# Performance work log

Measured on AMD Instinct MI355X. Metric: run time of the kernel, lower is better.

The kernel has to match this reference:

```python
import jax, jax.numpy as jnp
import numpy as np

LABEL_SIZE = 32
HIDDEN = 1024
TARGET = 1  # args.target
N_EVENTS = 4096
N_SIM = 4096


def setup_inputs() -> dict:
    key = jax.random.key(0)
    ks = jax.random.split(key, 10)
    L, H, n, n_sim = LABEL_SIZE, HIDDEN, N_EVENTS, N_SIM
    label_seq = jax.random.randint(ks[0], (n,), 0, L + 1)
    # strictly increasing event times (positive gaps)
    gaps = jax.random.uniform(ks[1], (n,), minval=0.01, maxval=1.0)
    time_seq = jnp.cumsum(gaps)
    sim_time_idx = jax.random.randint(ks[2], (n_sim,), 0, n - 1)
    sim_time_seq = time_seq[sim_time_idx] + jax.random.uniform(ks[3], (n_sim,), minval=0.0, maxval=0.5)
    stdv = 1.0 / np.sqrt(H)
    u = lambda k, shape: jax.random.uniform(k, shape, minval=-stdv, maxval=stdv)
    Emb = u(ks[4], (H, L + 1))
    W = u(ks[5], (7, H, H))
    U = u(ks[6], (7, H, H))
    d = jnp.zeros((7, H), dtype=jnp.float32)
    w = u(ks[7], (L, H))
    log_s = jnp.zeros((L,), dtype=jnp.float32)
    return {"label_seq": label_seq, "time_seq": time_seq, "sim_time_seq": sim_time_seq,
            "sim_time_idx": sim_time_idx, "ignore_first": 1,
            "Emb": Emb, "W": W, "U": U, "d": d, "w": w, "log_s": log_s}


def _neg_loglik(label_seq, time_seq, sim_time_seq, sim_time_idx, ignore_first,
                Emb, W, U, d, w, log_s):
    H = Emb.shape[0]
    tgt = TARGET
    emb = Emb[:, label_seq].T              # (n, H) event-label embeddings
    # Precompute input-to-gate projections for all steps: W @ label_prev
    Wx = jnp.einsum('ehk,nk->neh', W, emb[:-1])   # (n-1, 7, H)
    dts = time_seq[1:] - time_seq[:-1]            # (n-1,)

    def step(carry, inp):
        c_t, h_t, c_bar = carry
        wx, dt = inp
        temp = wx + jnp.einsum('ehk,k->eh', U, h_t) + d   # (7, H)
        i_g = jax.nn.sigmoid(temp[0])
        f_g = jax.nn.sigmoid(temp[1])
        z = jnp.tanh(temp[2])
        o = jax.nn.sigmoid(temp[3])
        i_b = jax.nn.sigmoid(temp[4])
        f_b = jax.nn.sigmoid(temp[5])
        delta = jax.nn.softplus(temp[6])
        c = f_g * c_t + i_g * z
        c_bar_n = f_b * c_bar + i_b * z
        c_t_n = c_bar_n + (c - c_bar_n) * jnp.exp(-delta * dt)
        h_n = o * jnp.tanh(c_t_n)
        return (c_t_n, h_n, c_bar_n), (h_n, c_bar_n, c, delta, o)

    z0 = jnp.zeros((H,), dtype=time_seq.dtype)
    _, (all_h, all_cbar, all_c, all_delta, all_o) = jax.lax.scan(step, (z0, z0, z0), (Wx, dts))

    def h_to_lambd(h):
        s = jnp.exp(log_s)
        return s * jax.nn.softplus((h @ w.T) / s) + 1e-9

    beg = 1 if ignore_first else 0
    h_evt = all_h[beg:-1]                               # (n-2-beg, H)
    lambd = h_to_lambd(h_evt)                           # (n-2-beg, L)
    mask = label_seq[1 + beg:-1] == tgt
    term1 = jnp.sum(jnp.where(mask, jnp.log(lambd[:, tgt - 1]), 0.0))

    decay = jnp.exp(-all_delta[sim_time_idx] * (sim_time_seq - time_seq[sim_time_idx])[:, None])
    c_sim = all_cbar[sim_time_idx] + (all_c[sim_time_idx] - all_cbar[sim_time_idx]) * decay
    h_sim = all_o[sim_time_idx] * jnp.tanh(c_sim)
    lambd_sim = h_to_lambd(h_sim)
    term2 = jnp.mean(lambd_sim[:, tgt - 1]) * (time_seq[-1] - time_seq[0])
    return -(term1 - term2)


def reference(label_seq, time_seq, sim_time_seq, sim_time_idx, ignore_first, Emb, W, U, d, w, log_s):
    return _neg_loglik(label_seq, time_seq, sim_time_seq, sim_time_idx, ignore_first,
                       Emb, W, U, d, w, log_s)
```

## Files before the change

kernel.cpp:

```cpp
#include <hip/hip_runtime.h>
#include <math.h>

#define H      1024
#define LBLP1  33
#define NE     4096
#define NS     4096
#define NSTEP  (NE - 1)
#define TGT    1
#define NWG    256
#define UPW    4
#define ROWS   28
#define SCAN_THREADS 512
#define SENTINEL 0xFFFFFFFFu

__device__ __forceinline__ float wave_sum(float v) {
#pragma unroll
    for (int o = 32; o > 0; o >>= 1) v += __shfl_xor(v, o, 64);
    return v;
}

__device__ __forceinline__ float softplusf(float x) {
    return x > 0.f ? x + log1pf(expf(-x)) : log1pf(expf(x));
}
__device__ __forceinline__ float sigmoidf(float x) {
    return 1.f / (1.f + expf(-x));
}

__global__ void embT_kernel(const float* __restrict__ Emb, float* __restrict__ EmbT) {
    int l = blockIdx.x;
    for (int k = threadIdx.x; k < H; k += blockDim.x)
        EmbT[(size_t)l * H + k] = Emb[(size_t)k * LBLP1 + l];
}

__global__ void wemb_kernel(const float* __restrict__ W, const float* __restrict__ EmbT,
                            const float* __restrict__ dbias, float* __restrict__ WEmb) {
    int row  = blockIdx.x;
    int wave = threadIdx.x >> 6;
    int lane = threadIdx.x & 63;
    __shared__ float wrow[H];
    for (int i = threadIdx.x; i < H; i += blockDim.x) wrow[i] = W[(size_t)row * H + i];
    __syncthreads();
    float db = dbias[row];
    for (int l = wave; l < LBLP1; l += 4) {
        const float* ec = EmbT + (size_t)l * H;
        float a = 0.f;
#pragma unroll
        for (int m = 0; m < 16; ++m) {
            int k = lane + (m << 6);
            a = fmaf(wrow[k], ec[k], a);
        }
        a = wave_sum(a);
        if (lane == 0) WEmb[(size_t)row * LBLP1 + l] = a + db;
    }
}

__global__ __launch_bounds__(SCAN_THREADS)
void scan_kernel(const float* __restrict__ WEmb, const float* __restrict__ U,
                 const int* __restrict__ label_seq, const float* __restrict__ time_seq,
                 float* __restrict__ all_h, float* __restrict__ all_o,
                 float* __restrict__ all_cb, float* __restrict__ all_cc,
                 float* __restrict__ all_dl) {
    const int tid  = threadIdx.x;
    const int wg   = blockIdx.x;
    const int wave = tid >> 6;
    const int lane = tid & 63;

    extern __shared__ float smem[];
    float* Uld    = smem;
    float* h_sh   = Uld + ROWS * H;
    float* act_sh = h_sh + H;
    float* wes    = act_sh + 32;

    for (int idx = tid; idx < ROWS * H; idx += SCAN_THREADS) {
        int r = idx >> 10, k = idx & (H - 1);
        int e = r >> 2, j = r & 3;
        Uld[idx] = U[((size_t)e * H + (wg * UPW + j)) * H + k];
    }
    for (int idx = tid; idx < ROWS * LBLP1; idx += SCAN_THREADS) {
        int r = idx / LBLP1, l = idx - r * LBLP1;
        int e = r >> 2, j = r & 3;
        wes[idx] = WEmb[((size_t)e * H + (wg * UPW + j)) * LBLP1 + l];
    }
    __syncthreads();

    float c_t = 0.f, cbar = 0.f;
    const float4* h4 = (const float4*)h_sh;

    for (int t = 0; t < NSTEP; ++t) {
        const int   lab = label_seq[t];
        const float dt  = time_seq[t + 1] - time_seq[t];
        float gb[4];
#pragma unroll
        for (int i = 0; i < 4; ++i) {
            int r = wave + (i << 3);
            gb[i] = (r < ROWS) ? wes[r * LBLP1 + lab] : 0.f;
        }

        if (wave == 0) {
            union { unsigned u[16]; float4 f[4]; } cv;
            if (t > 0) {
                const unsigned* src =
                    (const unsigned*)(all_h + (size_t)(t - 1) * H) + (lane << 4);
                for (;;) {
                    bool ok = true;
#pragma unroll
                    for (int j = 0; j < 16; ++j)
                        cv.u[j] = __hip_atomic_load(src + j, __ATOMIC_RELAXED,
                                                    __HIP_MEMORY_SCOPE_AGENT);
#pragma unroll
                    for (int j = 0; j < 16; ++j) ok &= (cv.u[j] != SENTINEL);
                    if (ok) break;
                }
            } else {
#pragma unroll
                for (int j = 0; j < 4; ++j) cv.f[j] = make_float4(0.f, 0.f, 0.f, 0.f);
            }
            float4* dst = (float4*)h_sh + (lane << 2);
#pragma unroll
            for (int j = 0; j < 4; ++j) dst[j] = cv.f[j];
        }
        __syncthreads();

        float4 hr[4];
#pragma unroll
        for (int m = 0; m < 4; ++m) hr[m] = h4[(m << 6) + lane];

#pragma unroll
        for (int i = 0; i < 4; ++i) {
            int r = wave + (i << 3);
            if (r < ROWS) {
                const float4* u4 = (const float4*)(Uld + (r << 10));
                float a = 0.f;
#pragma unroll
                for (int m = 0; m < 4; ++m) {
                    float4 u = u4[(m << 6) + lane];
                    a = fmaf(u.x, hr[m].x, a); a = fmaf(u.y, hr[m].y, a);
                    a = fmaf(u.z, hr[m].z, a); a = fmaf(u.w, hr[m].w, a);
                }
                a = wave_sum(a);
                if (lane == 0) {
                    float g = gb[i] + a;
                    int e = r >> 2;
                    float act;
                    if (e == 2)      act = tanhf(g);
                    else if (e == 6) act = softplusf(g);
                    else             act = sigmoidf(g);
                    act_sh[r] = act;
                }
            }
        }
        __syncthreads();

        if (tid < UPW) {
            float i_g = act_sh[tid],      f_g = act_sh[4 + tid];
            float z   = act_sh[8 + tid],  o   = act_sh[12 + tid];
            float i_b = act_sh[16 + tid], f_b = act_sh[20 + tid];
            float dl  = act_sh[24 + tid];
            float c   = fmaf(f_g, c_t, i_g * z);
            float cbn = fmaf(f_b, cbar, i_b * z);
            float ctn = cbn + (c - cbn) * expf(-dl * dt);
            float hn  = o * tanhf(ctn);
            c_t = ctn; cbar = cbn;
            size_t p = (size_t)t * H + wg * UPW + tid;
            __hip_atomic_store(&all_h[p], hn, __ATOMIC_RELAXED, __HIP_MEMORY_SCOPE_AGENT);
            all_o [p] = o;
            all_cb[p] = cbn;
            all_cc[p] = c;
            all_dl[p] = dl;
        }
    }
}

__global__ void term1_kernel(const float* __restrict__ all_h, const int* __restrict__ label_seq,
                             const float* __restrict__ w, const float* __restrict__ log_s,
                             const int* __restrict__ ignore_first, float* __restrict__ acc) {
    int beg = (*ignore_first) ? 1 : 0;
    int j = blockIdx.x;
    if (j >= (NSTEP - 1 - beg)) return;
    if (label_seq[1 + beg + j] != TGT) return;
    const float* hrow = all_h + (size_t)(beg + j) * H;
    const float* w0 = w + (TGT - 1) * H;
    float part = 0.f;
    for (int i = threadIdx.x; i < H; i += blockDim.x) part += hrow[i] * w0[i];
    __shared__ float red[4];
    part = wave_sum(part);
    if ((threadIdx.x & 63) == 0) red[threadIdx.x >> 6] = part;
    __syncthreads();
    if (threadIdx.x == 0) {
        float tot = red[0] + red[1] + red[2] + red[3];
        float s0 = expf(log_s[TGT - 1]);
        float lam = s0 * softplusf(tot / s0) + 1e-9f;
        atomicAdd(acc, logf(lam));
    }
}

__global__ void term2_kernel(const float* __restrict__ all_o, const float* __restrict__ all_cb,
                             const float* __restrict__ all_cc, const float* __restrict__ all_dl,
                             const int* __restrict__ sim_idx, const float* __restrict__ sim_time,
                             const float* __restrict__ time_seq, const float* __restrict__ w,
                             const float* __restrict__ log_s, float* __restrict__ acc) {
    int i = blockIdx.x;
    int idx = sim_idx[i];
    float dtp = sim_time[i] - time_seq[idx];
    size_t base = (size_t)idx * H;
    const float* w0 = w + (TGT - 1) * H;
    float part = 0.f;
    for (int hh = threadIdx.x; hh < H; hh += blockDim.x) {
        float cb = all_cb[base + hh];
        float cc = all_cc[base + hh];
        float dl = all_dl[base + hh];
        float oo = all_o [base + hh];
        float cs = cb + (cc - cb) * expf(-dl * dtp);
        part += oo * tanhf(cs) * w0[hh];
    }
    __shared__ float red[4];
    part = wave_sum(part);
    if ((threadIdx.x & 63) == 0) red[threadIdx.x >> 6] = part;
    __syncthreads();
    if (threadIdx.x == 0) {
        float tot = red[0] + red[1] + red[2] + red[3];
        float s0 = expf(log_s[TGT - 1]);
        float lam = s0 * softplusf(tot / s0) + 1e-9f;
        atomicAdd(acc + 1, lam);
    }
}

__global__ void finish_kernel(const float* __restrict__ acc, const float* __restrict__ time_seq,
                              float* __restrict__ out) {
    float T = time_seq[NE - 1] - time_seq[0];
    out[0] = -(acc[0] - acc[1] * (T / (float)NS));
}

extern "C" void kernel_launch(void* const* d_in, const int* in_sizes, int n_in,
                              void* d_out, int out_size, void* d_ws, size_t ws_size,
                              hipStream_t stream) {
    const int*   label_seq    = (const int*)  d_in[0];
    const float* time_seq     = (const float*)d_in[1];
    const float* sim_time     = (const float*)d_in[2];
    const int*   sim_idx      = (const int*)  d_in[3];
    const int*   ignore_first = (const int*)  d_in[4];
    const float* Emb   = (const float*)d_in[5];
    const float* W     = (const float*)d_in[6];
    const float* U     = (const float*)d_in[7];
    const float* dbias = (const float*)d_in[8];
    const float* w     = (const float*)d_in[9];
    const float* log_s = (const float*)d_in[10];
    float* out = (float*)d_out;

    float* ws = (float*)d_ws;
    size_t off = 0;
    float* acc    = ws + off;  off += 32;
    float* EmbT   = ws + off;  off += (size_t)LBLP1 * H;
    float* WEmb   = ws + off;  off += 7 * H * LBLP1;
    off = (off + 3) & ~(size_t)3;
    float* all_h  = ws + off;  off += (size_t)NSTEP * H;
    float* all_o  = ws + off;  off += (size_t)NSTEP * H;
    float* all_cb = ws + off;  off += (size_t)NSTEP * H;
    float* all_cc = ws + off;  off += (size_t)NSTEP * H;
    float* all_dl = ws + off;  off += (size_t)NSTEP * H;

    hipMemsetAsync(acc, 0, 2 * sizeof(float), stream);
    hipMemsetAsync(all_h, 0xFF, (size_t)NSTEP * H * sizeof(float), stream);

    hipLaunchKernelGGL(embT_kernel, dim3(LBLP1), dim3(256), 0, stream, Emb, EmbT);
    hipLaunchKernelGGL(wemb_kernel, dim3(7 * H), dim3(256), 0, stream,
                       W, EmbT, dbias, WEmb);

    unsigned int smem_bytes = (unsigned int)((ROWS * H + H + 32 + ROWS * LBLP1) * sizeof(float));
    hipFuncSetAttribute((const void*)scan_kernel, hipFuncAttributeMaxDynamicSharedMemorySize,
                        (int)smem_bytes);
    void* args[] = { (void*)&WEmb, (void*)&U, (void*)&label_seq, (void*)&time_seq,
                     (void*)&all_h, (void*)&all_o, (void*)&all_cb, (void*)&all_cc,
                     (void*)&all_dl };
    hipLaunchCooperativeKernel((void*)scan_kernel, dim3(NWG), dim3(SCAN_THREADS),
                               args, smem_bytes, stream);

    hipLaunchKernelGGL(term1_kernel, dim3(NSTEP - 1), dim3(256), 0, stream,
                       all_h, label_seq, w, log_s, ignore_first, acc);
    hipLaunchKernelGGL(term2_kernel, dim3(NS), dim3(256), 0, stream,
                       all_o, all_cb, all_cc, all_dl, sim_idx, sim_time, time_seq, w, log_s, acc);
    hipLaunchKernelGGL(finish_kernel, dim3(1), dim3(1), 0, stream, acc, time_seq, out);
}
```

Before: 19.36 ms.

## Exchange hidden state as replicated bf16 copies with one row per wave

The scan kernel now publishes each step's hidden state as packed bf16 into four replicated buffers, so groups of 64 workgroups poll separate copies. This halves the polling traffic and spreads contention across memory locations. Blocks grow to 1024 threads so each wave handles two gate rows instead of up to four, which shortens the per-step dot-product critical path. The bf16 rounding of the recurrent h input adds precision loss that accumulates over the 4095-step recurrence.

```diff
diff --git a/kernel.cpp b/kernel.cpp
--- a/kernel.cpp
+++ b/kernel.cpp
@@ -10,8 +10,9 @@
 #define NWG    256
 #define UPW    4
 #define ROWS   28
-#define SCAN_THREADS 512
-#define SENTINEL 0xFFFFFFFFu
+#define THREADS 1024
+#define NCPY   4
+#define SENT   0xFFFFFFFFu
 
 __device__ __forceinline__ float wave_sum(float v) {
 #pragma unroll
@@ -24,6 +25,11 @@
 }
 __device__ __forceinline__ float sigmoidf(float x) {
     return 1.f / (1.f + expf(-x));
+}
+
+__device__ __forceinline__ unsigned short f2bf(float f) {
+    unsigned u = __float_as_uint(f);
+    return (unsigned short)((u + 0x7FFFu + ((u >> 16) & 1u)) >> 16);
 }
 
 __global__ void embT_kernel(const float* __restrict__ Emb, float* __restrict__ EmbT) {
@@ -54,9 +60,10 @@
     }
 }
 
-__global__ __launch_bounds__(SCAN_THREADS)
+__global__ __launch_bounds__(THREADS)
 void scan_kernel(const float* __restrict__ WEmb, const float* __restrict__ U,
                  const int* __restrict__ label_seq, const float* __restrict__ time_seq,
+                 unsigned short* __restrict__ hcp,
                  float* __restrict__ all_h, float* __restrict__ all_o,
                  float* __restrict__ all_cb, float* __restrict__ all_cc,
                  float* __restrict__ all_dl) {
@@ -64,6 +71,7 @@
     const int wg   = blockIdx.x;
     const int wave = tid >> 6;
     const int lane = tid & 63;
+    const int mycopy = wg >> 6;
 
     extern __shared__ float smem[];
     float* Uld    = smem;
@@ -71,12 +79,12 @@
     float* act_sh = h_sh + H;
     float* wes    = act_sh + 32;
 
-    for (int idx = tid; idx < ROWS * H; idx += SCAN_THREADS) {
+    for (int idx = tid; idx < ROWS * H; idx += THREADS) {
         int r = idx >> 10, k = idx & (H - 1);
         int e = r >> 2, j = r & 3;
         Uld[idx] = U[((size_t)e * H + (wg * UPW + j)) * H + k];
     }
-    for (int idx = tid; idx < ROWS * LBLP1; idx += SCAN_THREADS) {
+    for (int idx = tid; idx < ROWS * LBLP1; idx += THREADS) {
         int r = idx / LBLP1, l = idx - r * LBLP1;
         int e = r >> 2, j = r & 3;
         wes[idx] = WEmb[((size_t)e * H + (wg * UPW + j)) * LBLP1 + l];
@@ -89,46 +97,52 @@
     for (int t = 0; t < NSTEP; ++t) {
         const int   lab = label_seq[t];
         const float dt  = time_seq[t + 1] - time_seq[t];
-        float gb[4];
-#pragma unroll
-        for (int i = 0; i < 4; ++i) {
-            int r = wave + (i << 3);
-            gb[i] = (r < ROWS) ? wes[r * LBLP1 + lab] : 0.f;
+
+        float gb0 = 0.f, gb1 = 0.f;
+        int r0 = (wave - 2) << 1;
+        if (wave >= 2) {
+            gb0 = wes[r0 * LBLP1 + lab];
+            gb1 = wes[(r0 + 1) * LBLP1 + lab];
         }
 
         if (wave == 0) {
-            union { unsigned u[16]; float4 f[4]; } cv;
+            unsigned v[8];
             if (t > 0) {
-                const unsigned* src =
-                    (const unsigned*)(all_h + (size_t)(t - 1) * H) + (lane << 4);
+                const unsigned* src = (const unsigned*)
+                    (hcp + ((size_t)mycopy * NSTEP + (t - 1)) * H);
                 for (;;) {
                     bool ok = true;
 #pragma unroll
-                    for (int j = 0; j < 16; ++j)
-                        cv.u[j] = __hip_atomic_load(src + j, __ATOMIC_RELAXED,
-                                                    __HIP_MEMORY_SCOPE_AGENT);
-#pragma unroll
-                    for (int j = 0; j < 16; ++j) ok &= (cv.u[j] != SENTINEL);
+                    for (int j = 0; j < 8; ++j)
+                        v[j] = __hip_atomic_load(src + (j << 6) + lane,
+                                                 __ATOMIC_RELAXED, __HIP_MEMORY_SCOPE_AGENT);
+#pragma unroll
+                    for (int j = 0; j < 8; ++j) ok &= (v[j] != SENT);
                     if (ok) break;
                 }
             } else {
 #pragma unroll
-                for (int j = 0; j < 4; ++j) cv.f[j] = make_float4(0.f, 0.f, 0.f, 0.f);
+                for (int j = 0; j < 8; ++j) v[j] = 0;
             }
-            float4* dst = (float4*)h_sh + (lane << 2);
-#pragma unroll
-            for (int j = 0; j < 4; ++j) dst[j] = cv.f[j];
+#pragma unroll
+            for (int j = 0; j < 8; ++j) {
+                float2 f2;
+                if (t > 0) {
+                    f2.x = __uint_as_float(v[j] << 16);
+                    f2.y = __uint_as_float(v[j] & 0xFFFF0000u);
+                } else f2 = make_float2(0.f, 0.f);
+                ((float2*)h_sh)[(j << 6) + lane] = f2;
+            }
         }
         __syncthreads();
 
-        float4 hr[4];
-#pragma unroll
-        for (int m = 0; m < 4; ++m) hr[m] = h4[(m << 6) + lane];
-
-#pragma unroll
-        for (int i = 0; i < 4; ++i) {
-            int r = wave + (i << 3);
-            if (r < ROWS) {
+        if (wave >= 2) {
+            float4 hr[4];
+#pragma unroll
+            for (int m = 0; m < 4; ++m) hr[m] = h4[(m << 6) + lane];
+#pragma unroll
+            for (int i = 0; i < 2; ++i) {
+                int r = r0 + i;
                 const float4* u4 = (const float4*)(Uld + (r << 10));
                 float a = 0.f;
 #pragma unroll
@@ -138,15 +152,13 @@
                     a = fmaf(u.z, hr[m].z, a); a = fmaf(u.w, hr[m].w, a);
                 }
                 a = wave_sum(a);
-                if (lane == 0) {
-                    float g = gb[i] + a;
-                    int e = r >> 2;
-                    float act;
-                    if (e == 2)      act = tanhf(g);
-                    else if (e == 6) act = softplusf(g);
-                    else             act = sigmoidf(g);
-                    act_sh[r] = act;
-                }
+                float g = (i ? gb1 : gb0) + a;
+                int e = r >> 2;
+                float act;
+                if (e == 2)      act = tanhf(g);
+                else if (e == 6) act = softplusf(g);
+                else             act = sigmoidf(g);
+                if (lane == 0) act_sh[r] = act;
             }
         }
         __syncthreads();
@@ -162,11 +174,26 @@
             float hn  = o * tanhf(ctn);
             c_t = ctn; cbar = cbn;
             size_t p = (size_t)t * H + wg * UPW + tid;
-            __hip_atomic_store(&all_h[p], hn, __ATOMIC_RELAXED, __HIP_MEMORY_SCOPE_AGENT);
+            all_h [p] = hn;
             all_o [p] = o;
             all_cb[p] = cbn;
             all_cc[p] = c;
             all_dl[p] = dl;
+            float h0 = __shfl(hn, 0), h1 = __shfl(hn, 1);
+            float h2 = __shfl(hn, 2), h3 = __shfl(hn, 3);
+            if (tid == 0) {
+                unsigned long long pk =
+                    (unsigned long long)f2bf(h0)
+                  | ((unsigned long long)f2bf(h1) << 16)
+                  | ((unsigned long long)f2bf(h2) << 32)
+                  | ((unsigned long long)f2bf(h3) << 48);
+                unsigned long long* base = (unsigned long long*)hcp;
+#pragma unroll
+                for (int cdst = 0; cdst < NCPY; ++cdst) {
+                    __hip_atomic_store(base + ((size_t)cdst * NSTEP + t) * (H / 4) + wg,
+                                       pk, __ATOMIC_RELAXED, __HIP_MEMORY_SCOPE_AGENT);
+                }
+            }
         }
     }
 }
@@ -258,9 +285,11 @@
     float* all_cb = ws + off;  off += (size_t)NSTEP * H;
     float* all_cc = ws + off;  off += (size_t)NSTEP * H;
     float* all_dl = ws + off;  off += (size_t)NSTEP * H;
+    unsigned short* hcp = (unsigned short*)(ws + off);
+    off += (size_t)NCPY * NSTEP * H / 2;
 
     hipMemsetAsync(acc, 0, 2 * sizeof(float), stream);
-    hipMemsetAsync(all_h, 0xFF, (size_t)NSTEP * H * sizeof(float), stream);
+    hipMemsetAsync(hcp, 0xFF, (size_t)NCPY * NSTEP * H * sizeof(unsigned short), stream);
 
     hipLaunchKernelGGL(embT_kernel, dim3(LBLP1), dim3(256), 0, stream, Emb, EmbT);
     hipLaunchKernelGGL(wemb_kernel, dim3(7 * H), dim3(256), 0, stream,
@@ -270,9 +299,9 @@
     hipFuncSetAttribute((const void*)scan_kernel, hipFuncAttributeMaxDynamicSharedMemorySize,
                         (int)smem_bytes);
     void* args[] = { (void*)&WEmb, (void*)&U, (void*)&label_seq, (void*)&time_seq,
-                     (void*)&all_h, (void*)&all_o, (void*)&all_cb, (void*)&all_cc,
-                     (void*)&all_dl };
-    hipLaunchCooperativeKernel((void*)scan_kernel, dim3(NWG), dim3(SCAN_THREADS),
+                     (void*)&hcp, (void*)&all_h, (void*)&all_o, (void*)&all_cb,
+                     (void*)&all_cc, (void*)&all_dl };
+    hipLaunchCooperativeKernel((void*)scan_kernel, dim3(NWG), dim3(THREADS),
                                args, smem_bytes, stream);
 
     hipLaunchKernelGGL(term1_kernel, dim3(NSTEP - 1), dim3(256), 0, stream,
```

After: 16.36 ms. -15.5%, faster.

## Pack U to fp16 and use tagged double-buffered h publication across 64 workgroups

Applied to the files above, without the earlier changes.

The recurrent weight U is converted to packed fp16 so each 64-workgroup × 16-wave scan keeps its rows partly in LDS and partly in registers, using fdot2 for the matvec. h is published as fp16 with a step tag in a small double-buffered, replicated mailbox instead of a sentinel-filled full history. This removes the large sentinel memset and cuts per-step cross-workgroup traffic and LDS footprint. The cost is reduced precision in the recurrent matvec and h exchange, which may drift over 4095 steps.

```diff
diff --git a/kernel.cpp b/kernel.cpp
--- a/kernel.cpp
+++ b/kernel.cpp
@@ -1,4 +1,5 @@
 #include <hip/hip_runtime.h>
+#include <hip/hip_fp16.h>
 #include <math.h>
 
 #define H      1024
@@ -7,23 +8,41 @@
 #define NS     4096
 #define NSTEP  (NE - 1)
 #define TGT    1
-#define NWG    256
-#define UPW    4
-#define ROWS   28
-#define SCAN_THREADS 512
-#define SENTINEL 0xFFFFFFFFu
+#define NWG    64
+#define UPW    16
+#define THREADS 1024
+#define NCPY   4
 
 __device__ __forceinline__ float wave_sum(float v) {
 #pragma unroll
     for (int o = 32; o > 0; o >>= 1) v += __shfl_xor(v, o, 64);
     return v;
 }
-
 __device__ __forceinline__ float softplusf(float x) {
     return x > 0.f ? x + log1pf(expf(-x)) : log1pf(expf(x));
 }
 __device__ __forceinline__ float sigmoidf(float x) {
     return 1.f / (1.f + expf(-x));
+}
+
+#if __has_builtin(__builtin_amdgcn_cvt_pkrtz) && __has_builtin(__builtin_amdgcn_fdot2)
+using half2_t = decltype(__builtin_amdgcn_cvt_pkrtz(0.f, 0.f));
+__device__ __forceinline__ float dot2(unsigned u, unsigned h, float c) {
+    return __builtin_amdgcn_fdot2(__builtin_bit_cast(half2_t, u),
+                                  __builtin_bit_cast(half2_t, h), c, false);
+}
+#else
+__device__ __forceinline__ float dot2(unsigned u, unsigned h, float c) {
+    float2 fa = __half22float2(__builtin_bit_cast(__half2, u));
+    float2 fb = __half22float2(__builtin_bit_cast(__half2, h));
+    c = fmaf(fa.x, fb.x, c);
+    c = fmaf(fa.y, fb.y, c);
+    return c;
+}
+#endif
+
+__device__ __forceinline__ unsigned pkhalf2(float a, float b) {
+    return __builtin_bit_cast(unsigned, __floats2half2_rn(a, b));
 }
 
 __global__ void embT_kernel(const float* __restrict__ Emb, float* __restrict__ EmbT) {
@@ -54,9 +73,20 @@
     }
 }
 
-__global__ __launch_bounds__(SCAN_THREADS)
-void scan_kernel(const float* __restrict__ WEmb, const float* __restrict__ U,
+__global__ void upk_kernel(const float* __restrict__ U, unsigned* __restrict__ Upk) {
+    int row = blockIdx.x;
+    const float4* src = (const float4*)(U + (size_t)row * H);
+    uint2* dst = (uint2*)(Upk + (size_t)row * (H / 2));
+    for (int j = threadIdx.x; j < H / 4; j += blockDim.x) {
+        float4 f = src[j];
+        dst[j] = make_uint2(pkhalf2(f.x, f.y), pkhalf2(f.z, f.w));
+    }
+}
+
+__global__ __launch_bounds__(THREADS)
+void scan_kernel(const unsigned* __restrict__ Upk, const float* __restrict__ WEmb,
                  const int* __restrict__ label_seq, const float* __restrict__ time_seq,
+                 unsigned* __restrict__ hpub,
                  float* __restrict__ all_h, float* __restrict__ all_o,
                  float* __restrict__ all_cb, float* __restrict__ all_cc,
                  float* __restrict__ all_dl) {
@@ -64,109 +94,130 @@
     const int wg   = blockIdx.x;
     const int wave = tid >> 6;
     const int lane = tid & 63;
-
-    extern __shared__ float smem[];
-    float* Uld    = smem;
-    float* h_sh   = Uld + ROWS * H;
-    float* act_sh = h_sh + H;
-    float* wes    = act_sh + 32;
-
-    for (int idx = tid; idx < ROWS * H; idx += SCAN_THREADS) {
-        int r = idx >> 10, k = idx & (H - 1);
-        int e = r >> 2, j = r & 3;
-        Uld[idx] = U[((size_t)e * H + (wg * UPW + j)) * H + k];
-    }
-    for (int idx = tid; idx < ROWS * LBLP1; idx += SCAN_THREADS) {
-        int r = idx / LBLP1, l = idx - r * LBLP1;
-        int e = r >> 2, j = r & 3;
-        wes[idx] = WEmb[((size_t)e * H + (wg * UPW + j)) * LBLP1 + l];
-    }
+    const int u    = wg * UPW + wave;
+
+    extern __shared__ unsigned smem_u[];
+    unsigned* uld  = smem_u;
+    unsigned* h_pk = uld + 64 * 512;
+    float*    wes  = (float*)(h_pk + 512);
+    float*    wscr = wes + 112 * LBLP1;
+
+#pragma unroll
+    for (int e = 0; e < 4; ++e)
+#pragma unroll
+        for (int m = 0; m < 8; ++m)
+            uld[(wave * 4 + e) * 512 + lane + (m << 6)] =
+                Upk[((size_t)e * H + u) * 512 + lane + (m << 6)];
+    unsigned ureg[3][8];
+#pragma unroll
+    for (int e = 0; e < 3; ++e)
+#pragma unroll
+        for (int m = 0; m < 8; ++m)
+            ureg[e][m] = Upk[((size_t)(4 + e) * H + u) * 512 + lane + (m << 6)];
+#pragma unroll
+    for (int g = 0; g < 7; ++g)
+        if (lane < LBLP1)
+            wes[(wave * 7 + g) * LBLP1 + lane] = WEmb[((size_t)g * H + u) * LBLP1 + lane];
     __syncthreads();
 
     float c_t = 0.f, cbar = 0.f;
-    const float4* h4 = (const float4*)h_sh;
 
     for (int t = 0; t < NSTEP; ++t) {
         const int   lab = label_seq[t];
         const float dt  = time_seq[t + 1] - time_seq[t];
-        float gb[4];
-#pragma unroll
-        for (int i = 0; i < 4; ++i) {
-            int r = wave + (i << 3);
-            gb[i] = (r < ROWS) ? wes[r * LBLP1 + lab] : 0.f;
-        }
 
         if (wave == 0) {
-            union { unsigned u[16]; float4 f[4]; } cv;
+            unsigned v[16];
             if (t > 0) {
-                const unsigned* src =
-                    (const unsigned*)(all_h + (size_t)(t - 1) * H) + (lane << 4);
+                const unsigned* src = hpub + (wg >> 4) * 2048 + (t & 1) * 1024 + lane;
                 for (;;) {
                     bool ok = true;
 #pragma unroll
                     for (int j = 0; j < 16; ++j)
-                        cv.u[j] = __hip_atomic_load(src + j, __ATOMIC_RELAXED,
-                                                    __HIP_MEMORY_SCOPE_AGENT);
-#pragma unroll
-                    for (int j = 0; j < 16; ++j) ok &= (cv.u[j] != SENTINEL);
-                    if (ok) break;
+                        v[j] = __hip_atomic_load(src + (j << 6), __ATOMIC_RELAXED,
+                                                 __HIP_MEMORY_SCOPE_AGENT);
+#pragma unroll
+                    for (int j = 0; j < 16; ++j) ok &= ((v[j] >> 16) == (unsigned)t);
+                    if (__all(ok)) break;
                 }
             } else {
 #pragma unroll
-                for (int j = 0; j < 4; ++j) cv.f[j] = make_float4(0.f, 0.f, 0.f, 0.f);
+                for (int j = 0; j < 16; ++j) v[j] = 0u;
             }
-            float4* dst = (float4*)h_sh + (lane << 2);
-#pragma unroll
-            for (int j = 0; j < 4; ++j) dst[j] = cv.f[j];
+#pragma unroll
+            for (int j = 0; j < 16; ++j) {
+                unsigned vx = __shfl_xor(v[j], 1, 64);
+                if ((lane & 1) == 0)
+                    h_pk[(j << 5) + (lane >> 1)] = (v[j] & 0xFFFFu) | (vx << 16);
+            }
         }
         __syncthreads();
 
-        float4 hr[4];
-#pragma unroll
-        for (int m = 0; m < 4; ++m) hr[m] = h4[(m << 6) + lane];
-
-#pragma unroll
-        for (int i = 0; i < 4; ++i) {
-            int r = wave + (i << 3);
-            if (r < ROWS) {
-                const float4* u4 = (const float4*)(Uld + (r << 10));
-                float a = 0.f;
-#pragma unroll
-                for (int m = 0; m < 4; ++m) {
-                    float4 u = u4[(m << 6) + lane];
-                    a = fmaf(u.x, hr[m].x, a); a = fmaf(u.y, hr[m].y, a);
-                    a = fmaf(u.z, hr[m].z, a); a = fmaf(u.w, hr[m].w, a);
-                }
-                a = wave_sum(a);
-                if (lane == 0) {
-                    float g = gb[i] + a;
-                    int e = r >> 2;
-                    float act;
-                    if (e == 2)      act = tanhf(g);
-                    else if (e == 6) act = softplusf(g);
-                    else             act = sigmoidf(g);
-                    act_sh[r] = act;
-                }
-            }
-        }
-        __syncthreads();
-
-        if (tid < UPW) {
-            float i_g = act_sh[tid],      f_g = act_sh[4 + tid];
-            float z   = act_sh[8 + tid],  o   = act_sh[12 + tid];
-            float i_b = act_sh[16 + tid], f_b = act_sh[20 + tid];
-            float dl  = act_sh[24 + tid];
-            float c   = fmaf(f_g, c_t, i_g * z);
-            float cbn = fmaf(f_b, cbar, i_b * z);
+        unsigned hreg[8];
+#pragma unroll
+        for (int m = 0; m < 8; ++m) hreg[m] = h_pk[lane + (m << 6)];
+
+        float p[7];
+#pragma unroll
+        for (int e = 0; e < 4; ++e) {
+            float a = 0.f;
+#pragma unroll
+            for (int m = 0; m < 8; ++m)
+                a = dot2(uld[(wave * 4 + e) * 512 + lane + (m << 6)], hreg[m], a);
+            p[e] = a;
+        }
+#pragma unroll
+        for (int e = 0; e < 3; ++e) {
+            float a = 0.f;
+#pragma unroll
+            for (int m = 0; m < 8; ++m)
+                a = dot2(ureg[e][m], hreg[m], a);
+            p[4 + e] = a;
+        }
+#pragma unroll
+        for (int g = 0; g < 7; ++g) {
+            p[g] += __shfl_xor(p[g], 1, 64);
+            p[g] += __shfl_xor(p[g], 2, 64);
+            p[g] += __shfl_xor(p[g], 4, 64);
+        }
+        if ((lane & 7) == 0) {
+            int grp = lane >> 3;
+#pragma unroll
+            for (int g = 0; g < 7; ++g)
+                wscr[(wave << 6) + (grp << 3) + g] = p[g];
+        }
+        asm volatile("s_waitcnt lgkmcnt(0)" ::: "memory");
+
+        float act = 0.f;
+        if (lane < 7) {
+            float s = 0.f;
+#pragma unroll
+            for (int k = 0; k < 8; ++k) s += wscr[(wave << 6) + (k << 3) + lane];
+            float g = s + wes[(wave * 7 + lane) * LBLP1 + lab];
+            act = (lane == 2) ? tanhf(g) : (lane == 6) ? softplusf(g) : sigmoidf(g);
+        }
+        float ig = __shfl(act, 0), fg = __shfl(act, 1), zz = __shfl(act, 2);
+        float oo = __shfl(act, 3), ib = __shfl(act, 4), fb = __shfl(act, 5);
+        float dl = __shfl(act, 6);
+
+        if (lane == 0) {
+            float c   = fmaf(fg, c_t, ig * zz);
+            float cbn = fmaf(fb, cbar, ib * zz);
             float ctn = cbn + (c - cbn) * expf(-dl * dt);
-            float hn  = o * tanhf(ctn);
+            float hn  = oo * tanhf(ctn);
             c_t = ctn; cbar = cbn;
-            size_t p = (size_t)t * H + wg * UPW + tid;
-            __hip_atomic_store(&all_h[p], hn, __ATOMIC_RELAXED, __HIP_MEMORY_SCOPE_AGENT);
-            all_o [p] = o;
-            all_cb[p] = cbn;
-            all_cc[p] = c;
-            all_dl[p] = dl;
+            unsigned pk = ((unsigned)(t + 1) << 16) | (pkhalf2(hn, 0.f) & 0xFFFFu);
+            int slotbase = ((t + 1) & 1) * 1024 + u;
+#pragma unroll
+            for (int cp = 0; cp < NCPY; ++cp)
+                __hip_atomic_store(&hpub[cp * 2048 + slotbase], pk,
+                                   __ATOMIC_RELAXED, __HIP_MEMORY_SCOPE_AGENT);
+            size_t pos = (size_t)t * H + u;
+            all_h [pos] = hn;
+            all_o [pos] = oo;
+            all_cb[pos] = cbn;
+            all_cc[pos] = c;
+            all_dl[pos] = dl;
         }
     }
 }
@@ -249,10 +300,12 @@
 
     float* ws = (float*)d_ws;
     size_t off = 0;
-    float* acc    = ws + off;  off += 32;
-    float* EmbT   = ws + off;  off += (size_t)LBLP1 * H;
-    float* WEmb   = ws + off;  off += 7 * H * LBLP1;
+    float*    acc  = ws + off;              off += 32;
+    float*    EmbT = ws + off;              off += (size_t)LBLP1 * H;
+    float*    WEmb = ws + off;              off += (size_t)7 * H * LBLP1;
     off = (off + 3) & ~(size_t)3;
+    unsigned* Upk  = (unsigned*)(ws + off); off += (size_t)7 * H * (H / 2);
+    unsigned* hpub = (unsigned*)(ws + off); off += (size_t)NCPY * 2048;
     float* all_h  = ws + off;  off += (size_t)NSTEP * H;
     float* all_o  = ws + off;  off += (size_t)NSTEP * H;
     float* all_cb = ws + off;  off += (size_t)NSTEP * H;
@@ -260,19 +313,21 @@
     float* all_dl = ws + off;  off += (size_t)NSTEP * H;
 
     hipMemsetAsync(acc, 0, 2 * sizeof(float), stream);
-    hipMemsetAsync(all_h, 0xFF, (size_t)NSTEP * H * sizeof(float), stream);
+    hipMemsetAsync(hpub, 0, (size_t)NCPY * 2048 * sizeof(unsigned), stream);
 
     hipLaunchKernelGGL(embT_kernel, dim3(LBLP1), dim3(256), 0, stream, Emb, EmbT);
     hipLaunchKernelGGL(wemb_kernel, dim3(7 * H), dim3(256), 0, stream,
                        W, EmbT, dbias, WEmb);
-
-    unsigned int smem_bytes = (unsigned int)((ROWS * H + H + 32 + ROWS * LBLP1) * sizeof(float));
+    hipLaunchKernelGGL(upk_kernel, dim3(7 * H), dim3(256), 0, stream, U, Upk);
+
+    unsigned int smem_bytes = (unsigned int)((64 * 512 + 512) * 4
+                                             + (112 * LBLP1 + 16 * 64) * 4);
     hipFuncSetAttribute((const void*)scan_kernel, hipFuncAttributeMaxDynamicSharedMemorySize,
                         (int)smem_bytes);
-    void* args[] = { (void*)&WEmb, (void*)&U, (void*)&label_seq, (void*)&time_seq,
-                     (void*)&all_h, (void*)&all_o, (void*)&all_cb, (void*)&all_cc,
-                     (void*)&all_dl };
-    hipLaunchCooperativeKernel((void*)scan_kernel, dim3(NWG), dim3(SCAN_THREADS),
+    void* args[] = { (void*)&Upk, (void*)&WEmb, (void*)&label_seq, (void*)&time_seq,
+                     (void*)&hpub, (void*)&all_h, (void*)&all_o, (void*)&all_cb,
+                     (void*)&all_cc, (void*)&all_dl };
+    hipLaunchCooperativeKernel((void*)scan_kernel, dim3(NWG), dim3(THREADS),
                                args, smem_bytes, stream);
 
     hipLaunchKernelGGL(term1_kernel, dim3(NSTEP - 1), dim3(256), 0, stream,
```

New measurement: 25.09 ms. 29.6% more time.
